# Kernel tuning notes

Measured on AMD Instinct MI355X. Metric: run time of the kernel, lower is better.

The kernel has to match this reference:

```python
import jax, jax.numpy as jnp
import numpy as np

INPUT_DIM = 256
RES_DIM = 2048
OUT_DIM = 256
BATCH = 32
SEQ = 512
LEAK = 0.3
TARGET_SR = 0.9
IN_CONN = 0.1
RES_CONN = 0.1
IN_SCALE = 1.0


def _make_params(seed=0):
    rng = np.random.default_rng(seed)
    W_in = rng.standard_normal((RES_DIM, INPUT_DIM)).astype(np.float32)
    W_in = W_in * (rng.random((RES_DIM, INPUT_DIM)) < IN_CONN).astype(np.float32) * IN_SCALE
    W = rng.standard_normal((RES_DIM, RES_DIM)).astype(np.float32)
    W = W * (rng.random((RES_DIM, RES_DIM)) < RES_CONN).astype(np.float32)
    sr = np.abs(np.linalg.eigvals(W.astype(np.float64))).max()
    if sr > 0:
        W = (W * (TARGET_SR / sr)).astype(np.float32)
    bias = np.zeros((RES_DIM,), np.float32)
    # readout Linear(reservoir_dim, output_dim), torch default init
    bound = 1.0 / np.sqrt(RES_DIM)
    w_ro = rng.uniform(-bound, bound, (OUT_DIM, RES_DIM)).astype(np.float32)
    b_ro = rng.uniform(-bound, bound, (OUT_DIM,)).astype(np.float32)
    return W_in, W, bias, w_ro, b_ro


def setup_inputs() -> dict:
    key = jax.random.key(0)
    k_u, _ = jax.random.split(key)
    u = jax.random.normal(k_u, (BATCH, SEQ, INPUT_DIM), dtype=jnp.float32)
    state = jnp.zeros((BATCH, RES_DIM), dtype=jnp.float32)
    W_in, W, bias, w_ro, b_ro = _make_params()
    return {
        'u': u,
        'state': state,
        'W_in': jnp.asarray(W_in),
        'W': jnp.asarray(W),
        'bias': jnp.asarray(bias),
        'w_ro': jnp.asarray(w_ro),
        'b_ro': jnp.asarray(b_ro),
    }


def reference(u, state, W_in, W, bias, w_ro, b_ro):
    # Precompute input projection for all timesteps in one GEMM: (T, B, R)
    u_proj = jnp.einsum('bti,ri->tbr', u, W_in) + bias

    def step(s, up):
        pre = up + s @ W.T            # (B, R)
        s = (1.0 - LEAK) * s + LEAK * jnp.tanh(pre)
        return s, s

    _, states = jax.lax.scan(step, state, u_proj)  # (T, B, R)
    states = jnp.transpose(states, (1, 0, 2))       # (B, T, R)
    output = jnp.einsum('btr,or->bto', states, w_ro) + b_ro
    return output
```

## Files before the change

kernel.cpp:

```cpp
#include <hip/hip_runtime.h>
#include <math.h>

#define BATCH 32
#define SEQ   512
#define IDIM  256
#define RDIM  2048
#define ODIM  256
#define LEAK  0.3f

#define SCAN_BLOCKS  256
#define SCAN_THREADS 512
#define ROWS_PER_BLK 8

typedef float f4 __attribute__((ext_vector_type(4)));

__device__ __forceinline__ unsigned ld_flag(const unsigned* p) {
    return __hip_atomic_load(p, __ATOMIC_RELAXED, __HIP_MEMORY_SCOPE_AGENT);
}
__device__ __forceinline__ void st_flag(unsigned* p, unsigned v) {
    __hip_atomic_store(p, v, __ATOMIC_RELAXED, __HIP_MEMORY_SCOPE_AGENT);
}

__global__ void esn_init(const float* __restrict__ s0, float* __restrict__ states,
                         unsigned* __restrict__ flags) {
    int idx = blockIdx.x * blockDim.x + threadIdx.x;
    const int n4 = (BATCH * RDIM) / 4;
    if (idx < n4) {
        ((float4*)states)[idx] = ((const float4*)s0)[idx];
    }
    if (idx < 1024) flags[idx] = 0u;
}

#define UP_THREADS 256
__global__ __launch_bounds__(UP_THREADS) void esn_uproj(
    const float* __restrict__ u,
    const float* __restrict__ Win,
    const float* __restrict__ bias,
    float* __restrict__ up)
{
    __shared__ float St[32][68];
    __shared__ float Wt[32][68];

    const int tid  = threadIdx.x;
    const int row0 = blockIdx.x * 64;
    const int o0   = blockIdx.y * 64;

    const int lr = tid >> 3;
    const int lk = (tid & 7) * 4;
    const int tx = tid & 15;
    const int ty = tid >> 4;

    const int m0 = row0 + lr;
    const int m1 = row0 + 32 + lr;
    const float* u0 = u + ((size_t)(m0 & 31) * SEQ + (m0 >> 5)) * IDIM;
    const float* u1 = u + ((size_t)(m1 & 31) * SEQ + (m1 >> 5)) * IDIM;

    float acc[4][4] = {};

    for (int kt = 0; kt < IDIM; kt += 32) {
        float4 a0 = *(const float4*)(u0 + kt + lk);
        float4 a1 = *(const float4*)(u1 + kt + lk);
        float4 w0 = *(const float4*)(Win + (size_t)(o0 + lr)      * IDIM + kt + lk);
        float4 w1 = *(const float4*)(Win + (size_t)(o0 + 32 + lr) * IDIM + kt + lk);
        __syncthreads();
        float av0[4] = {a0.x, a0.y, a0.z, a0.w};
        float av1[4] = {a1.x, a1.y, a1.z, a1.w};
        float wv0[4] = {w0.x, w0.y, w0.z, w0.w};
        float wv1[4] = {w1.x, w1.y, w1.z, w1.w};
        #pragma unroll
        for (int j = 0; j < 4; ++j) {
            St[lk + j][lr]      = av0[j];
            St[lk + j][32 + lr] = av1[j];
            Wt[lk + j][lr]      = wv0[j];
            Wt[lk + j][32 + lr] = wv1[j];
        }
        __syncthreads();
        #pragma unroll
        for (int k = 0; k < 32; ++k) {
            float4 a4 = *(const float4*)(&St[k][4 * ty]);
            float4 b4 = *(const float4*)(&Wt[k][4 * tx]);
            float av[4] = {a4.x, a4.y, a4.z, a4.w};
            float bv[4] = {b4.x, b4.y, b4.z, b4.w};
            #pragma unroll
            for (int ri = 0; ri < 4; ++ri)
                #pragma unroll
                for (int oi = 0; oi < 4; ++oi)
                    acc[ri][oi] += av[ri] * bv[oi];
        }
    }

    float4 bs = *(const float4*)(bias + o0 + 4 * tx);
    float bsv[4] = {bs.x, bs.y, bs.z, bs.w};
    #pragma unroll
    for (int ri = 0; ri < 4; ++ri) {
        int row = row0 + 4 * ty + ri;
        float4 v;
        v.x = acc[ri][0] + bsv[0];
        v.y = acc[ri][1] + bsv[1];
        v.z = acc[ri][2] + bsv[2];
        v.w = acc[ri][3] + bsv[3];
        *(float4*)(up + (size_t)row * RDIM + o0 + 4 * tx) = v;
    }
}

#define DECL_A(r)  float A##r##0 = 0.0f, A##r##1 = 0.0f, A##r##2 = 0.0f, A##r##3 = 0.0f;
#define ZERO_A(r)  A##r##0 = 0.0f; A##r##1 = 0.0f; A##r##2 = 0.0f; A##r##3 = 0.0f;
#define DOT_ROW(r) { f4 w = *(const f4*)(wl + (r) * RDIM); \
    A##r##0 += w[0]*SC0[0] + w[1]*SC0[1] + w[2]*SC0[2] + w[3]*SC0[3]; \
    A##r##1 += w[0]*SC1[0] + w[1]*SC1[1] + w[2]*SC1[2] + w[3]*SC1[3]; \
    A##r##2 += w[0]*SC2[0] + w[1]*SC2[1] + w[2]*SC2[2] + w[3]*SC2[3]; \
    A##r##3 += w[0]*SC3[0] + w[1]*SC3[1] + w[2]*SC3[2] + w[3]*SC3[3]; }
#define RED12(x)   { x += __shfl_xor(x, 1, 64); x += __shfl_xor(x, 2, 64); }
#define RED_A(r)   RED12(A##r##0) RED12(A##r##1) RED12(A##r##2) RED12(A##r##3)
#define COMPACT(r) float V##r; { \
    float x01 = (q & 1) ? A##r##1 : A##r##0; \
    float x23 = (q & 1) ? A##r##3 : A##r##2; \
    float v   = (q & 2) ? x23 : x01; \
    v += __shfl_xor(v, 4, 64);  v += __shfl_xor(v, 8, 64); \
    v += __shfl_xor(v, 16, 64); v += __shfl_xor(v, 32, 64); \
    V##r = v; }

__global__ __launch_bounds__(SCAN_THREADS) void esn_scan(
    const float* __restrict__ W,
    float* __restrict__ states,
    unsigned* __restrict__ flags)
{
    __shared__ float Wl[ROWS_PER_BLK * RDIM];
    __shared__ unsigned lcnt;

    const int tid  = threadIdx.x;
    const int bid  = blockIdx.x;
    const int r0   = bid * ROWS_PER_BLK;

    if (tid == 0) lcnt = 0u;

    {
        const float4* src = (const float4*)(W + (size_t)r0 * RDIM);
        float4* dst = (float4*)Wl;
        #pragma unroll
        for (int i = 0; i < (ROWS_PER_BLK * RDIM) / 4 / SCAN_THREADS; ++i)
            dst[i * SCAN_THREADS + tid] = src[i * SCAN_THREADS + tid];
    }

    const int wave = tid >> 6;
    const int lane = tid & 63;
    const int b0   = wave * 4;
    const int kb   = lane * 4;
    const int q    = lane & 3;

    const int bf = b0 + q;
    const int rr = lane >> 2;
    const size_t fin_off = (size_t)bf * RDIM + r0 + rr;

    unsigned* mygo = &flags[256 + (bid & 7) * 16];
    const bool is_agg = (bid == 0) && (wave == 0);

    float so = 0.0f;
    if (lane < 32) so = states[fin_off];

    DECL_A(0) DECL_A(1) DECL_A(2) DECL_A(3)
    DECL_A(4) DECL_A(5) DECL_A(6) DECL_A(7)

    __syncthreads();

    for (int t = 0; t < SEQ; ++t) {
        const float* prev = states + (size_t)t * (BATCH * RDIM);
        float* next = states + (size_t)(t + 1) * (BATCH * RDIM);

        float up = 0.0f;
        if (lane < 32)
            up = __hip_atomic_load(&next[fin_off], __ATOMIC_RELAXED,
                                   __HIP_MEMORY_SCOPE_AGENT);

        ZERO_A(0) ZERO_A(1) ZERO_A(2) ZERO_A(3)
        ZERO_A(4) ZERO_A(5) ZERO_A(6) ZERO_A(7)

        {
            const float* sb = prev + kb;
            f4 SC0 = *(const f4*)(sb + (size_t)(b0 + 0) * RDIM);
            f4 SC1 = *(const f4*)(sb + (size_t)(b0 + 1) * RDIM);
            f4 SC2 = *(const f4*)(sb + (size_t)(b0 + 2) * RDIM);
            f4 SC3 = *(const f4*)(sb + (size_t)(b0 + 3) * RDIM);

            #pragma unroll 1
            for (int c = 0; c < 8; ++c) {
                f4 SN0 = SC0, SN1 = SC1, SN2 = SC2, SN3 = SC3;
                if (c < 7) {
                    SN0 = *(const f4*)(sb + (size_t)(b0 + 0) * RDIM + (c + 1) * 256);
                    SN1 = *(const f4*)(sb + (size_t)(b0 + 1) * RDIM + (c + 1) * 256);
                    SN2 = *(const f4*)(sb + (size_t)(b0 + 2) * RDIM + (c + 1) * 256);
                    SN3 = *(const f4*)(sb + (size_t)(b0 + 3) * RDIM + (c + 1) * 256);
                }
                const float* wl = &Wl[c * 256 + kb];
                DOT_ROW(0) DOT_ROW(1) DOT_ROW(2) DOT_ROW(3)
                DOT_ROW(4) DOT_ROW(5) DOT_ROW(6) DOT_ROW(7)
                SC0 = SN0; SC1 = SN1; SC2 = SN2; SC3 = SN3;
            }
        }

        RED_A(0) RED_A(1) RED_A(2) RED_A(3)
        RED_A(4) RED_A(5) RED_A(6) RED_A(7)
        COMPACT(0) COMPACT(1) COMPACT(2) COMPACT(3)
        COMPACT(4) COMPACT(5) COMPACT(6) COMPACT(7)

        if (lane < 32) {
            float pre = V0;
            if (rr == 1) pre = V1;
            if (rr == 2) pre = V2;
            if (rr == 3) pre = V3;
            if (rr == 4) pre = V4;
            if (rr == 5) pre = V5;
            if (rr == 6) pre = V6;
            if (rr == 7) pre = V7;
            pre += up;
            float sn = (1.0f - LEAK) * so + LEAK * tanhf(pre);
            so = sn;
            __hip_atomic_store(&next[fin_off], sn,
                               __ATOMIC_RELAXED, __HIP_MEMORY_SCOPE_AGENT);
        }

        asm volatile("s_waitcnt vmcnt(0)" ::: "memory");
        const unsigned tp = (unsigned)(t + 1);
        if (lane == 0) __hip_atomic_fetch_add(&lcnt, 1u, __ATOMIC_RELAXED,
                                              __HIP_MEMORY_SCOPE_WORKGROUP);

        if (wave == 0) {
            if (lane == 0) {
                while (__hip_atomic_load(&lcnt, __ATOMIC_RELAXED,
                                         __HIP_MEMORY_SCOPE_WORKGROUP) < 8u * tp)
                    __builtin_amdgcn_s_sleep(1);
                st_flag(&flags[bid], tp);
            }
            if (is_agg) {
                for (;;) {
                    unsigned f0 = ld_flag(&flags[lane]);
                    unsigned f1 = ld_flag(&flags[64 + lane]);
                    unsigned f2 = ld_flag(&flags[128 + lane]);
                    unsigned f3 = ld_flag(&flags[192 + lane]);
                    bool ok = (f0 >= tp) & (f1 >= tp) & (f2 >= tp) & (f3 >= tp);
                    if (__all(ok)) break;
                    __builtin_amdgcn_s_sleep(1);
                }
                asm volatile("" ::: "memory");
                if (lane < 8) st_flag(&flags[256 + lane * 16], tp);
                asm volatile("s_waitcnt vmcnt(0)" ::: "memory");
                continue;
            }
        }

        while (ld_flag(mygo) < tp) __builtin_amdgcn_s_sleep(1);
        asm volatile("" ::: "memory");
    }
}

#define RO_THREADS 256
__global__ __launch_bounds__(RO_THREADS) void esn_readout(
    const float* __restrict__ states,
    const float* __restrict__ w_ro,
    const float* __restrict__ b_ro,
    float* __restrict__ out)
{
    __shared__ float St[32][68];
    __shared__ float Wt[32][68];

    const int tid  = threadIdx.x;
    const int rb   = blockIdx.x >> 2;
    const int ob   = blockIdx.x & 3;
    const int row0 = rb * 64;
    const int o0   = ob * 64;
    const float* S = states + (size_t)BATCH * RDIM;

    const int lr = tid >> 3;
    const int lk = (tid & 7) * 4;
    const int tx = tid & 15;
    const int ty = tid >> 4;

    float acc[4][4] = {};

    for (int kt = 0; kt < RDIM; kt += 32) {
        float4 a0 = *(const float4*)(S + (size_t)(row0 + lr)      * RDIM + kt + lk);
        float4 a1 = *(const float4*)(S + (size_t)(row0 + 32 + lr) * RDIM + kt + lk);
        float4 w0 = *(const float4*)(w_ro + (size_t)(o0 + lr)      * RDIM + kt + lk);
        float4 w1 = *(const float4*)(w_ro + (size_t)(o0 + 32 + lr) * RDIM + kt + lk);
        __syncthreads();
        float av0[4] = {a0.x, a0.y, a0.z, a0.w};
        float av1[4] = {a1.x, a1.y, a1.z, a1.w};
        float wv0[4] = {w0.x, w0.y, w0.z, w0.w};
        float wv1[4] = {w1.x, w1.y, w1.z, w1.w};
        #pragma unroll
        for (int j = 0; j < 4; ++j) {
            St[lk + j][lr]      = av0[j];
            St[lk + j][32 + lr] = av1[j];
            Wt[lk + j][lr]      = wv0[j];
            Wt[lk + j][32 + lr] = wv1[j];
        }
        __syncthreads();
        #pragma unroll
        for (int k = 0; k < 32; ++k) {
            float4 a4 = *(const float4*)(&St[k][4 * ty]);
            float4 b4 = *(const float4*)(&Wt[k][4 * tx]);
            float av[4] = {a4.x, a4.y, a4.z, a4.w};
            float bv[4] = {b4.x, b4.y, b4.z, b4.w};
            #pragma unroll
            for (int ri = 0; ri < 4; ++ri)
                #pragma unroll
                for (int oi = 0; oi < 4; ++oi)
                    acc[ri][oi] += av[ri] * bv[oi];
        }
    }

    float4 br = *(const float4*)(b_ro + o0 + 4 * tx);
    float brv[4] = {br.x, br.y, br.z, br.w};
    #pragma unroll
    for (int ri = 0; ri < 4; ++ri) {
        int row = row0 + 4 * ty + ri;
        int tt  = row >> 5;
        int bbx = row & 31;
        float4 v;
        v.x = acc[ri][0] + brv[0];
        v.y = acc[ri][1] + brv[1];
        v.z = acc[ri][2] + brv[2];
        v.w = acc[ri][3] + brv[3];
        *(float4*)(out + ((size_t)bbx * SEQ + tt) * ODIM + o0 + 4 * tx) = v;
    }
}

extern "C" void kernel_launch(void* const* d_in, const int* in_sizes, int n_in,
                              void* d_out, int out_size, void* d_ws, size_t ws_size,
                              hipStream_t stream) {
    const float* u    = (const float*)d_in[0];
    const float* s0   = (const float*)d_in[1];
    const float* Win  = (const float*)d_in[2];
    const float* W    = (const float*)d_in[3];
    const float* bias = (const float*)d_in[4];
    const float* w_ro = (const float*)d_in[5];
    const float* b_ro = (const float*)d_in[6];
    float* out = (float*)d_out;

    const size_t states_elems = (size_t)(SEQ + 1) * BATCH * RDIM;
    const size_t states_bytes = states_elems * sizeof(float);
    const size_t need = states_bytes + 4096;
    if (ws_size < need) return;

    float* states = (float*)d_ws;
    unsigned* flags = (unsigned*)((char*)d_ws + states_bytes);

    esn_init<<<dim3(64), dim3(256), 0, stream>>>(s0, states, flags);

    esn_uproj<<<dim3((SEQ * BATCH) / 64, RDIM / 64), dim3(UP_THREADS), 0, stream>>>(
        u, Win, bias, states + (size_t)BATCH * RDIM);

    void* args[] = { (void*)&W, (void*)&states, (void*)&flags };
    hipLaunchCooperativeKernel((const void*)esn_scan,
                               dim3(SCAN_BLOCKS), dim3(SCAN_THREADS),
                               args, 0, stream);

    esn_readout<<<dim3((SEQ * BATCH / 64) * (ODIM / 64)), dim3(RO_THREADS), 0, stream>>>(
        states, w_ro, b_ro, out);
}
```

Measured before the change: 4.820 ms.

## Use split-bf16 MFMA for the recurrent matvec with hi/lo state planes

The scan kernel's per-step state-times-W product moves from FP32 FMA dot products with shuffle reductions to bf16 MFMA 16x16x32 instructions. Each value is split into hi and lo bf16 parts and three MFMAs approximate fp32 accuracy. States and input projections are stored as two bf16 planes instead of fp32, and K-split partial sums are reduced through shared memory. This cuts vector ALU work and shuffle traffic per step, at the cost of an extra __syncthreads per step, split/recombine overhead, and a small precision loss from dropping the lo*lo term.

```diff
diff --git a/kernel.cpp b/kernel.cpp
--- a/kernel.cpp
+++ b/kernel.cpp
@@ -11,8 +11,12 @@
 #define SCAN_BLOCKS  256
 #define SCAN_THREADS 512
 #define ROWS_PER_BLK 8
-
-typedef float f4 __attribute__((ext_vector_type(4)));
+#define WSTRIDE      2056
+#define SLOT         (BATCH * RDIM)
+
+typedef float          f4  __attribute__((ext_vector_type(4)));
+typedef short          s8v __attribute__((ext_vector_type(8)));
+typedef unsigned short u4v __attribute__((ext_vector_type(4)));
 
 __device__ __forceinline__ unsigned ld_flag(const unsigned* p) {
     return __hip_atomic_load(p, __ATOMIC_RELAXED, __HIP_MEMORY_SCOPE_AGENT);
@@ -20,13 +24,30 @@
 __device__ __forceinline__ void st_flag(unsigned* p, unsigned v) {
     __hip_atomic_store(p, v, __ATOMIC_RELAXED, __HIP_MEMORY_SCOPE_AGENT);
 }
-
-__global__ void esn_init(const float* __restrict__ s0, float* __restrict__ states,
+__device__ __forceinline__ float bf2f(unsigned short h) {
+    return __builtin_bit_cast(float, (unsigned)h << 16);
+}
+__device__ __forceinline__ void split_bf16(float x, unsigned short& hi,
+                                           unsigned short& lo) {
+    unsigned u = __builtin_bit_cast(unsigned, x);
+    unsigned r = u + 0x7FFFu + ((u >> 16) & 1u);
+    hi = (unsigned short)(r >> 16);
+    float rem = x - bf2f(hi);
+    unsigned ul = __builtin_bit_cast(unsigned, rem);
+    unsigned rl = ul + 0x7FFFu + ((ul >> 16) & 1u);
+    lo = (unsigned short)(rl >> 16);
+}
+
+__global__ void esn_init(const float* __restrict__ s0,
+                         unsigned short* __restrict__ shi,
+                         unsigned short* __restrict__ slo,
                          unsigned* __restrict__ flags) {
     int idx = blockIdx.x * blockDim.x + threadIdx.x;
-    const int n4 = (BATCH * RDIM) / 4;
-    if (idx < n4) {
-        ((float4*)states)[idx] = ((const float4*)s0)[idx];
+    if (idx < SLOT) {
+        unsigned short h, l;
+        split_bf16(s0[idx], h, l);
+        shi[idx] = h;
+        slo[idx] = l;
     }
     if (idx < 1024) flags[idx] = 0u;
 }
@@ -36,7 +57,8 @@
     const float* __restrict__ u,
     const float* __restrict__ Win,
     const float* __restrict__ bias,
-    float* __restrict__ up)
+    unsigned short* __restrict__ uphi,
+    unsigned short* __restrict__ uplo)
 {
     __shared__ float St[32][68];
     __shared__ float Wt[32][68];
@@ -94,150 +116,157 @@
     #pragma unroll
     for (int ri = 0; ri < 4; ++ri) {
         int row = row0 + 4 * ty + ri;
-        float4 v;
-        v.x = acc[ri][0] + bsv[0];
-        v.y = acc[ri][1] + bsv[1];
-        v.z = acc[ri][2] + bsv[2];
-        v.w = acc[ri][3] + bsv[3];
-        *(float4*)(up + (size_t)row * RDIM + o0 + 4 * tx) = v;
-    }
-}
-
-#define DECL_A(r)  float A##r##0 = 0.0f, A##r##1 = 0.0f, A##r##2 = 0.0f, A##r##3 = 0.0f;
-#define ZERO_A(r)  A##r##0 = 0.0f; A##r##1 = 0.0f; A##r##2 = 0.0f; A##r##3 = 0.0f;
-#define DOT_ROW(r) { f4 w = *(const f4*)(wl + (r) * RDIM); \
-    A##r##0 += w[0]*SC0[0] + w[1]*SC0[1] + w[2]*SC0[2] + w[3]*SC0[3]; \
-    A##r##1 += w[0]*SC1[0] + w[1]*SC1[1] + w[2]*SC1[2] + w[3]*SC1[3]; \
-    A##r##2 += w[0]*SC2[0] + w[1]*SC2[1] + w[2]*SC2[2] + w[3]*SC2[3]; \
-    A##r##3 += w[0]*SC3[0] + w[1]*SC3[1] + w[2]*SC3[2] + w[3]*SC3[3]; }
-#define RED12(x)   { x += __shfl_xor(x, 1, 64); x += __shfl_xor(x, 2, 64); }
-#define RED_A(r)   RED12(A##r##0) RED12(A##r##1) RED12(A##r##2) RED12(A##r##3)
-#define COMPACT(r) float V##r; { \
-    float x01 = (q & 1) ? A##r##1 : A##r##0; \
-    float x23 = (q & 1) ? A##r##3 : A##r##2; \
-    float v   = (q & 2) ? x23 : x01; \
-    v += __shfl_xor(v, 4, 64);  v += __shfl_xor(v, 8, 64); \
-    v += __shfl_xor(v, 16, 64); v += __shfl_xor(v, 32, 64); \
-    V##r = v; }
-
-__global__ __launch_bounds__(SCAN_THREADS) void esn_scan(
+        unsigned short h0, l0, h1, l1, h2, l2, h3, l3;
+        split_bf16(acc[ri][0] + bsv[0], h0, l0);
+        split_bf16(acc[ri][1] + bsv[1], h1, l1);
+        split_bf16(acc[ri][2] + bsv[2], h2, l2);
+        split_bf16(acc[ri][3] + bsv[3], h3, l3);
+        u4v hv = {h0, h1, h2, h3};
+        u4v lv = {l0, l1, l2, l3};
+        *(u4v*)(uphi + (size_t)row * RDIM + o0 + 4 * tx) = hv;
+        *(u4v*)(uplo + (size_t)row * RDIM + o0 + 4 * tx) = lv;
+    }
+}
+
+__global__ __launch_bounds__(SCAN_THREADS)
+__attribute__((amdgpu_waves_per_eu(2, 2)))
+void esn_scan(
     const float* __restrict__ W,
-    float* __restrict__ states,
+    unsigned short* __restrict__ shi,
+    unsigned short* __restrict__ slo,
     unsigned* __restrict__ flags)
 {
-    __shared__ float Wl[ROWS_PER_BLK * RDIM];
+    __shared__ unsigned short WhiL[16 * WSTRIDE];
+    __shared__ unsigned short WloL[16 * WSTRIDE];
+    __shared__ float part[4 * 256];
     __shared__ unsigned lcnt;
 
-    const int tid  = threadIdx.x;
-    const int bid  = blockIdx.x;
-    const int r0   = bid * ROWS_PER_BLK;
-
+    const int tid = threadIdx.x;
+    const int bid = blockIdx.x;
+    const int r0  = bid * ROWS_PER_BLK;
     if (tid == 0) lcnt = 0u;
 
-    {
-        const float4* src = (const float4*)(W + (size_t)r0 * RDIM);
-        float4* dst = (float4*)Wl;
-        #pragma unroll
-        for (int i = 0; i < (ROWS_PER_BLK * RDIM) / 4 / SCAN_THREADS; ++i)
-            dst[i * SCAN_THREADS + tid] = src[i * SCAN_THREADS + tid];
-    }
-
-    const int wave = tid >> 6;
-    const int lane = tid & 63;
-    const int b0   = wave * 4;
-    const int kb   = lane * 4;
-    const int q    = lane & 3;
-
-    const int bf = b0 + q;
-    const int rr = lane >> 2;
-    const size_t fin_off = (size_t)bf * RDIM + r0 + rr;
+    for (int r = 0; r < 16; ++r) {
+        for (int k = tid; k < RDIM; k += SCAN_THREADS) {
+            unsigned short h = 0, l = 0;
+            if (r < 8) split_bf16(W[(size_t)(r0 + r) * RDIM + k], h, l);
+            WhiL[r * WSTRIDE + k] = h;
+            WloL[r * WSTRIDE + k] = l;
+        }
+    }
+
+    const int wave  = tid >> 6;
+    const int lane  = tid & 63;
+    const int quad  = lane >> 4;
+    const int mn    = lane & 15;
+    const int mtile = wave & 1;
+    const int kg    = wave >> 1;
+
+    const int aoff = (mtile * 16 + mn) * RDIM + kg * 512 + quad * 8;
+    const unsigned short* pbh = &WhiL[mn * WSTRIDE + kg * 512 + quad * 8];
+    const unsigned short* pbl = &WloL[mn * WSTRIDE + kg * 512 + quad * 8];
+
+    const int bf   = tid >> 2;
+    const int rn0  = (tid & 3) * 2;
+    const int fin0 = bf * RDIM + r0 + rn0;
+
+    float so0 = 0.0f, so1 = 0.0f;
+    if (tid < 128) {
+        so0 = bf2f(shi[fin0])     + bf2f(slo[fin0]);
+        so1 = bf2f(shi[fin0 + 1]) + bf2f(slo[fin0 + 1]);
+    }
 
     unsigned* mygo = &flags[256 + (bid & 7) * 16];
     const bool is_agg = (bid == 0) && (wave == 0);
 
-    float so = 0.0f;
-    if (lane < 32) so = states[fin_off];
-
-    DECL_A(0) DECL_A(1) DECL_A(2) DECL_A(3)
-    DECL_A(4) DECL_A(5) DECL_A(6) DECL_A(7)
-
     __syncthreads();
 
     for (int t = 0; t < SEQ; ++t) {
-        const float* prev = states + (size_t)t * (BATCH * RDIM);
-        float* next = states + (size_t)(t + 1) * (BATCH * RDIM);
-
-        float up = 0.0f;
-        if (lane < 32)
-            up = __hip_atomic_load(&next[fin_off], __ATOMIC_RELAXED,
-                                   __HIP_MEMORY_SCOPE_AGENT);
-
-        ZERO_A(0) ZERO_A(1) ZERO_A(2) ZERO_A(3)
-        ZERO_A(4) ZERO_A(5) ZERO_A(6) ZERO_A(7)
-
+        const size_t bprev = (size_t)t * SLOT;
+        const size_t bnext = bprev + SLOT;
+        const unsigned tp = (unsigned)(t + 1);
+
+        unsigned uph = 0, upl = 0;
+        if (tid < 128) {
+            uph = __hip_atomic_load((const unsigned*)(shi + bnext + fin0),
+                                    __ATOMIC_RELAXED, __HIP_MEMORY_SCOPE_AGENT);
+            upl = __hip_atomic_load((const unsigned*)(slo + bnext + fin0),
+                                    __ATOMIC_RELAXED, __HIP_MEMORY_SCOPE_AGENT);
+        }
+
+        f4 acc = {0.0f, 0.0f, 0.0f, 0.0f};
         {
-            const float* sb = prev + kb;
-            f4 SC0 = *(const f4*)(sb + (size_t)(b0 + 0) * RDIM);
-            f4 SC1 = *(const f4*)(sb + (size_t)(b0 + 1) * RDIM);
-            f4 SC2 = *(const f4*)(sb + (size_t)(b0 + 2) * RDIM);
-            f4 SC3 = *(const f4*)(sb + (size_t)(b0 + 3) * RDIM);
-
+            const unsigned short* pah = shi + bprev + aoff;
+            const unsigned short* pal = slo + bprev + aoff;
+            s8v AH = *(const s8v*)pah;
+            s8v AL = *(const s8v*)pal;
+            s8v BH = *(const s8v*)pbh;
+            s8v BL = *(const s8v*)pbl;
             #pragma unroll 1
-            for (int c = 0; c < 8; ++c) {
-                f4 SN0 = SC0, SN1 = SC1, SN2 = SC2, SN3 = SC3;
-                if (c < 7) {
-                    SN0 = *(const f4*)(sb + (size_t)(b0 + 0) * RDIM + (c + 1) * 256);
-                    SN1 = *(const f4*)(sb + (size_t)(b0 + 1) * RDIM + (c + 1) * 256);
-                    SN2 = *(const f4*)(sb + (size_t)(b0 + 2) * RDIM + (c + 1) * 256);
-                    SN3 = *(const f4*)(sb + (size_t)(b0 + 3) * RDIM + (c + 1) * 256);
+            for (int tk = 0; tk < 16; ++tk) {
+                s8v AH2 = AH, AL2 = AL, BH2 = BH, BL2 = BL;
+                if (tk < 15) {
+                    AH2 = *(const s8v*)(pah + (tk + 1) * 32);
+                    AL2 = *(const s8v*)(pal + (tk + 1) * 32);
+                    BH2 = *(const s8v*)(pbh + (tk + 1) * 32);
+                    BL2 = *(const s8v*)(pbl + (tk + 1) * 32);
                 }
-                const float* wl = &Wl[c * 256 + kb];
-                DOT_ROW(0) DOT_ROW(1) DOT_ROW(2) DOT_ROW(3)
-                DOT_ROW(4) DOT_ROW(5) DOT_ROW(6) DOT_ROW(7)
-                SC0 = SN0; SC1 = SN1; SC2 = SN2; SC3 = SN3;
+                acc = __builtin_amdgcn_mfma_f32_16x16x32_bf16(AH, BH, acc, 0, 0, 0);
+                acc = __builtin_amdgcn_mfma_f32_16x16x32_bf16(AL, BH, acc, 0, 0, 0);
+                acc = __builtin_amdgcn_mfma_f32_16x16x32_bf16(AH, BL, acc, 0, 0, 0);
+                AH = AH2; AL = AL2; BH = BH2; BL = BL2;
             }
         }
 
-        RED_A(0) RED_A(1) RED_A(2) RED_A(3)
-        RED_A(4) RED_A(5) RED_A(6) RED_A(7)
-        COMPACT(0) COMPACT(1) COMPACT(2) COMPACT(3)
-        COMPACT(4) COMPACT(5) COMPACT(6) COMPACT(7)
-
-        if (lane < 32) {
-            float pre = V0;
-            if (rr == 1) pre = V1;
-            if (rr == 2) pre = V2;
-            if (rr == 3) pre = V3;
-            if (rr == 4) pre = V4;
-            if (rr == 5) pre = V5;
-            if (rr == 6) pre = V6;
-            if (rr == 7) pre = V7;
-            pre += up;
-            float sn = (1.0f - LEAK) * so + LEAK * tanhf(pre);
-            so = sn;
-            __hip_atomic_store(&next[fin_off], sn,
+        if (mn < 8) {
+            const int pb = kg * 256 + (mtile * 16 + quad * 4) * 8 + mn;
+            part[pb]      = acc[0];
+            part[pb + 8]  = acc[1];
+            part[pb + 16] = acc[2];
+            part[pb + 24] = acc[3];
+        }
+        __syncthreads();
+
+        if (tid < 128) {
+            const int pi = bf * 8 + rn0;
+            float p0 = part[pi]     + part[256 + pi]     + part[512 + pi]     + part[768 + pi];
+            float p1 = part[pi + 1] + part[256 + pi + 1] + part[512 + pi + 1] + part[768 + pi + 1];
+            float up0 = bf2f((unsigned short)(uph & 0xFFFFu))
+                      + bf2f((unsigned short)(upl & 0xFFFFu));
+            float up1 = bf2f((unsigned short)(uph >> 16))
+                      + bf2f((unsigned short)(upl >> 16));
+            float sn0 = (1.0f - LEAK) * so0 + LEAK * tanhf(p0 + up0);
+            float sn1 = (1.0f - LEAK) * so1 + LEAK * tanhf(p1 + up1);
+            so0 = sn0; so1 = sn1;
+            unsigned short h0, l0, h1, l1;
+            split_bf16(sn0, h0, l0);
+            split_bf16(sn1, h1, l1);
+            __hip_atomic_store((unsigned*)(shi + bnext + fin0),
+                               (unsigned)h0 | ((unsigned)h1 << 16),
                                __ATOMIC_RELAXED, __HIP_MEMORY_SCOPE_AGENT);
-        }
-
-        asm volatile("s_waitcnt vmcnt(0)" ::: "memory");
-        const unsigned tp = (unsigned)(t + 1);
-        if (lane == 0) __hip_atomic_fetch_add(&lcnt, 1u, __ATOMIC_RELAXED,
-                                              __HIP_MEMORY_SCOPE_WORKGROUP);
+            __hip_atomic_store((unsigned*)(slo + bnext + fin0),
+                               (unsigned)l0 | ((unsigned)l1 << 16),
+                               __ATOMIC_RELAXED, __HIP_MEMORY_SCOPE_AGENT);
+            asm volatile("s_waitcnt vmcnt(0)" ::: "memory");
+            if (lane == 0)
+                __hip_atomic_fetch_add(&lcnt, 1u, __ATOMIC_RELAXED,
+                                       __HIP_MEMORY_SCOPE_WORKGROUP);
+        }
 
         if (wave == 0) {
             if (lane == 0) {
                 while (__hip_atomic_load(&lcnt, __ATOMIC_RELAXED,
-                                         __HIP_MEMORY_SCOPE_WORKGROUP) < 8u * tp)
+                                         __HIP_MEMORY_SCOPE_WORKGROUP) < 2u * tp)
                     __builtin_amdgcn_s_sleep(1);
                 st_flag(&flags[bid], tp);
             }
             if (is_agg) {
                 for (;;) {
-                    unsigned f0 = ld_flag(&flags[lane]);
-                    unsigned f1 = ld_flag(&flags[64 + lane]);
-                    unsigned f2 = ld_flag(&flags[128 + lane]);
-                    unsigned f3 = ld_flag(&flags[192 + lane]);
-                    bool ok = (f0 >= tp) & (f1 >= tp) & (f2 >= tp) & (f3 >= tp);
+                    unsigned g0 = ld_flag(&flags[lane]);
+                    unsigned g1 = ld_flag(&flags[64 + lane]);
+                    unsigned g2 = ld_flag(&flags[128 + lane]);
+                    unsigned g3 = ld_flag(&flags[192 + lane]);
+                    bool ok = (g0 >= tp) & (g1 >= tp) & (g2 >= tp) & (g3 >= tp);
                     if (__all(ok)) break;
                     __builtin_amdgcn_s_sleep(1);
                 }
@@ -247,7 +276,6 @@
                 continue;
             }
         }
-
         while (ld_flag(mygo) < tp) __builtin_amdgcn_s_sleep(1);
         asm volatile("" ::: "memory");
     }
@@ -255,7 +283,8 @@
 
 #define RO_THREADS 256
 __global__ __launch_bounds__(RO_THREADS) void esn_readout(
-    const float* __restrict__ states,
+    const unsigned short* __restrict__ shi,
+    const unsigned short* __restrict__ slo,
     const float* __restrict__ w_ro,
     const float* __restrict__ b_ro,
     float* __restrict__ out)
@@ -268,7 +297,8 @@
     const int ob   = blockIdx.x & 3;
     const int row0 = rb * 64;
     const int o0   = ob * 64;
-    const float* S = states + (size_t)BATCH * RDIM;
+    const unsigned short* Shi = shi + SLOT;
+    const unsigned short* Slo = slo + SLOT;
 
     const int lr = tid >> 3;
     const int lk = (tid & 7) * 4;
@@ -278,13 +308,17 @@
     float acc[4][4] = {};
 
     for (int kt = 0; kt < RDIM; kt += 32) {
-        float4 a0 = *(const float4*)(S + (size_t)(row0 + lr)      * RDIM + kt + lk);
-        float4 a1 = *(const float4*)(S + (size_t)(row0 + 32 + lr) * RDIM + kt + lk);
+        u4v h0 = *(const u4v*)(Shi + (size_t)(row0 + lr)      * RDIM + kt + lk);
+        u4v l0 = *(const u4v*)(Slo + (size_t)(row0 + lr)      * RDIM + kt + lk);
+        u4v h1 = *(const u4v*)(Shi + (size_t)(row0 + 32 + lr) * RDIM + kt + lk);
+        u4v l1 = *(const u4v*)(Slo + (size_t)(row0 + 32 + lr) * RDIM + kt + lk);
         float4 w0 = *(const float4*)(w_ro + (size_t)(o0 + lr)      * RDIM + kt + lk);
         float4 w1 = *(const float4*)(w_ro + (size_t)(o0 + 32 + lr) * RDIM + kt + lk);
         __syncthreads();
-        float av0[4] = {a0.x, a0.y, a0.z, a0.w};
-        float av1[4] = {a1.x, a1.y, a1.z, a1.w};
+        float av0[4] = {bf2f(h0[0]) + bf2f(l0[0]), bf2f(h0[1]) + bf2f(l0[1]),
+                        bf2f(h0[2]) + bf2f(l0[2]), bf2f(h0[3]) + bf2f(l0[3])};
+        float av1[4] = {bf2f(h1[0]) + bf2f(l1[0]), bf2f(h1[1]) + bf2f(l1[1]),
+                        bf2f(h1[2]) + bf2f(l1[2]), bf2f(h1[3]) + bf2f(l1[3])};
         float wv0[4] = {w0.x, w0.y, w0.z, w0.w};
         float wv1[4] = {w1.x, w1.y, w1.z, w1.w};
         #pragma unroll
@@ -337,24 +371,25 @@
     const float* b_ro = (const float*)d_in[6];
     float* out = (float*)d_out;
 
-    const size_t states_elems = (size_t)(SEQ + 1) * BATCH * RDIM;
-    const size_t states_bytes = states_elems * sizeof(float);
-    const size_t need = states_bytes + 4096;
+    const size_t plane_elems = (size_t)(SEQ + 1) * SLOT;
+    const size_t plane_bytes = plane_elems * sizeof(unsigned short);
+    const size_t need = 2 * plane_bytes + 4096;
     if (ws_size < need) return;
 
-    float* states = (float*)d_ws;
-    unsigned* flags = (unsigned*)((char*)d_ws + states_bytes);
-
-    esn_init<<<dim3(64), dim3(256), 0, stream>>>(s0, states, flags);
+    unsigned short* shi = (unsigned short*)d_ws;
+    unsigned short* slo = shi + plane_elems;
+    unsigned* flags = (unsigned*)((char*)d_ws + 2 * plane_bytes);
+
+    esn_init<<<dim3(256), dim3(256), 0, stream>>>(s0, shi, slo, flags);
 
     esn_uproj<<<dim3((SEQ * BATCH) / 64, RDIM / 64), dim3(UP_THREADS), 0, stream>>>(
-        u, Win, bias, states + (size_t)BATCH * RDIM);
-
-    void* args[] = { (void*)&W, (void*)&states, (void*)&flags };
+        u, Win, bias, shi + SLOT, slo + SLOT);
+
+    void* args[] = { (void*)&W, (void*)&shi, (void*)&slo, (void*)&flags };
     hipLaunchCooperativeKernel((const void*)esn_scan,
                                dim3(SCAN_BLOCKS), dim3(SCAN_THREADS),
                                args, 0, stream);
 
     esn_readout<<<dim3((SEQ * BATCH / 64) * (ODIM / 64)), dim3(RO_THREADS), 0, stream>>>(
-        states, w_ro, b_ro, out);
-}
+        shi, slo, w_ro, b_ro, out);
+}
```

Measured after the change: 5.629 ms. +16.8%, slower.
